# Kernel optimization log

Hardware: AMD Instinct MI355X
Metric: run time of the kernel (lower is better)

The kernel has to match this reference:

```python
import jax, jax.numpy as jnp
import numpy as np

LAM_FACE = 0.1
LAM_HAIR = 0.1
LAM_EYE = 0.1
NBINS = 256


def _denorm255(x):
    # de_norm: (x+1)/2 clamped to [0,1], then *255
    return jnp.clip((x + 1.0) * 0.5, 0.0, 1.0) * 255.0


def _labels_to_mask(m, vals):
    # sum of float indicators, matching (m==v).float() + ... in the original
    out = jnp.zeros(m.shape, jnp.float32)
    for v in vals:
        out = out + (m == v).astype(jnp.float32)
    return out


def _masked_cdf(img_masked, w):
    # img_masked: [3,H,W] values in [0,255] (already multiplied by mask)
    # w: [H,W] bool, one count per nonzero-mask pixel (mirrors mask.nonzero())
    # np.histogram(bins=256, range=(0,255)) -> bin = floor(v*256/255), last bin right-inclusive
    bins = jnp.clip(jnp.floor(img_masked * (256.0 / 255.0)), 0, NBINS - 1).astype(jnp.int32)
    wf = jnp.broadcast_to(w, img_masked.shape).astype(jnp.float32).reshape(3, -1)
    hist = jax.vmap(lambda b, ww: jax.ops.segment_sum(ww, b, num_segments=NBINS))(
        bins.reshape(3, -1), wf)  # [3,256]
    hist = hist / jnp.maximum(hist.sum(axis=1, keepdims=True), 1.0)
    return jnp.cumsum(hist, axis=1)


def _cal_trans(dc, ac):
    # table[i] = first j in 1..255 with dc[i] in [ac[j-1], ac[j]]; else i. table[0]=0, table[255]=255.
    cond = (dc[:, None] >= ac[None, :-1]) & (dc[:, None] <= ac[None, 1:])  # [256,255]
    found = jnp.any(cond, axis=1)
    j = jnp.argmax(cond, axis=1) + 1
    tbl = jnp.where(found, j, jnp.arange(NBINS))
    tbl = tbl.at[0].set(0).at[NBINS - 1].set(NBINS - 1)
    return tbl


def _region_loss(inp, tar, mask_src, mask_tar):
    # inp/tar: [3,H,W] denormed images; mask_*: [H,W] float indicator sums
    w_src = mask_src != 0
    w_tar = mask_tar != 0
    im = inp * mask_src[None]   # input_masked
    tm = tar * mask_tar[None]   # target_masked
    d = _masked_cdf(im, w_src)  # dst CDF per channel
    a = _masked_cdf(tm, w_tar)  # ref CDF per channel
    tables = jax.vmap(_cal_trans)(d, a)  # [3,256] int32
    idx = jnp.clip(im.astype(jnp.int32), 0, NBINS - 1)  # int(value), nonneg so trunc==floor
    looked = jnp.take_along_axis(tables, idx.reshape(3, -1), axis=1).reshape(im.shape)
    matched = jnp.where(w_src[None], looked.astype(im.dtype), im)
    matched = jax.lax.stop_gradient(matched)  # histogram_matching output is requires_grad=False
    return jnp.mean(jnp.abs(im - matched))   # L1Loss over [3,H,W]


def setup_inputs() -> dict:
    key = jax.random.key(0)
    k1, k2, k3, k4 = jax.random.split(key, 4)
    H = 2048
    fake_A = jax.random.normal(k1, (1, 3, H, H), dtype=jnp.float32)
    ref_B = jax.random.normal(k2, (1, 3, H, H), dtype=jnp.float32)
    mask_A = jax.random.randint(k3, (1, 1, H, H), 0, 19, dtype=jnp.int32)
    mask_B = jax.random.randint(k4, (1, 1, H, H), 0, 19, dtype=jnp.int32)
    return {"fake_A": fake_A, "ref_B": ref_B, "mask_A": mask_A, "mask_B": mask_B}


def reference(fake_A, ref_B, mask_A, mask_B):
    ma = mask_A[0, 0]
    mb = mask_B[0, 0]
    # region masks (note: original has a bug, mask_B_face uses (mask_A == 11); kept faithfully)
    mA_face = _labels_to_mask(ma, [1, 10, 14, 7, 8, 11])
    mB_face = _labels_to_mask(mb, [1, 10, 14, 7, 8]) + (ma == 11).astype(jnp.float32)
    mA_hair = _labels_to_mask(ma, [17])
    mB_hair = _labels_to_mask(mb, [17])
    mA_el = _labels_to_mask(ma, [4, 2])
    mA_er = _labels_to_mask(ma, [5, 3])
    mB_el = _labels_to_mask(mb, [4, 2])
    mB_er = _labels_to_mask(mb, [5, 3])
    inp = _denorm255(fake_A[0])
    tar = _denorm255(ref_B[0])
    loss = LAM_FACE * _region_loss(inp, tar, mA_face, mB_face)
    loss = loss + LAM_HAIR * _region_loss(inp, tar, mA_hair, mB_hair)
    loss = loss + LAM_EYE * (_region_loss(inp, tar, mA_el, mB_el)
                             + _region_loss(inp, tar, mA_er, mB_er))
    return loss
```

## Files before the change

kernel.cpp:

```cpp
#include <hip/hip_runtime.h>


typedef unsigned long long u64;
typedef long long s64;

#define NSRC 256
#define M41 ((1ull << 41) - 1)

static constexpr u64 REGA =
    (1ull << (3 * 1)) | (3ull << (3 * 2)) | (4ull << (3 * 3)) |
    (3ull << (3 * 4)) | (4ull << (3 * 5)) | (1ull << (3 * 7)) |
    (1ull << (3 * 8)) | (1ull << (3 * 10)) | (1ull << (3 * 11)) |
    (1ull << (3 * 14)) | (2ull << (3 * 17));
static constexpr u64 REGB =
    (1ull << (3 * 1)) | (3ull << (3 * 2)) | (4ull << (3 * 3)) |
    (3ull << (3 * 4)) | (4ull << (3 * 5)) | (1ull << (3 * 7)) |
    (1ull << (3 * 8)) | (1ull << (3 * 10)) | (1ull << (3 * 14)) |
    (2ull << (3 * 17));

__device__ __forceinline__ float denorm255(float x) {
  float t = (x + 1.0f) * 0.5f;
  t = fminf(fmaxf(t, 0.0f), 1.0f);
  return t * 255.0f;
}

__device__ __forceinline__ int bin_of(float v) {
  int b = (int)(v * (256.0f / 255.0f));
  return b > 255 ? 255 : b;
}

__global__ __launch_bounds__(1024, 8) void hm_kernel(
    const float* __restrict__ fake, const float* __restrict__ refb,
    const int* __restrict__ ma, const int* __restrict__ mb,
    u64* __restrict__ gNS, u64* __restrict__ gT,
    unsigned* __restrict__ ticket, unsigned* __restrict__ ticket2,
    u64* __restrict__ acc, float* __restrict__ out, int npix) {
  __shared__ u64 lds64[6144];
  const int tid = threadIdx.x;
  const int nq = npix >> 2;

  if (blockIdx.x < NSRC) {
    u64* ns = lds64;
    for (int i = tid; i < 6144; i += 1024) ns[i] = 0ull;
    __syncthreads();

    const float4* f0p = (const float4*)fake;
    const float4* f1p = (const float4*)(fake + npix);
    const float4* f2p = (const float4*)(fake + 2 * npix);
    const int4* map = (const int4*)ma;

    for (int q = blockIdx.x * 1024 + tid; q < nq; q += NSRC * 1024) {
      int4 m4 = map[q];
      float4 f0 = f0p[q], f1 = f1p[q], f2 = f2p[q];
      int mm[4] = {m4.x, m4.y, m4.z, m4.w};
      float fa[3][4] = {{f0.x, f0.y, f0.z, f0.w},
                        {f1.x, f1.y, f1.z, f1.w},
                        {f2.x, f2.y, f2.z, f2.w}};
#pragma unroll
      for (int k = 0; k < 4; ++k) {
        unsigned l = (unsigned)mm[k];
        int code = (int)((REGA >> (l + l + l)) & 7u);
        if (code) {
          int base = (code - 1) * 3;
#pragma unroll
          for (int c = 0; c < 3; ++c) {
            float v = denorm255(fa[c][k]);
            int key = (int)v + bin_of(v);
            u64 pack = (1ull << 41) | (u64)(unsigned)(v * 2048.0f);
            atomicAdd(&ns[(base + c) * 512 + key], pack);
          }
        }
      }
    }
    __syncthreads();

    int copy = blockIdx.x & 7;
    int rot = ((blockIdx.x >> 3) & 63) * 8;
    for (int i = tid; i < 6144; i += 1024) {
      int rc = i >> 9, key = ((i & 511) + rot) & 511;
      u64 v = ns[rc * 512 + key];
      if (v) atomicAdd(&gNS[copy * 6144 + rc * 512 + key], v);
    }
  } else {
    unsigned* th0 = (unsigned*)lds64;
    for (int i = tid; i < 12288; i += 1024) th0[i] = 0u;
    __syncthreads();
    unsigned* th = th0 + (tid >> 8) * 3072;

    const float4* r0p = (const float4*)refb;
    const float4* r1p = (const float4*)(refb + npix);
    const float4* r2p = (const float4*)(refb + 2 * npix);
    const int4* map = (const int4*)ma;
    const int4* mbp = (const int4*)mb;

    for (int q = (blockIdx.x - NSRC) * 1024 + tid; q < nq;
         q += (512 - NSRC) * 1024) {
      int4 ma4 = map[q], mb4 = mbp[q];
      float4 r0 = r0p[q], r1 = r1p[q], r2 = r2p[q];
      int mm[4] = {ma4.x, ma4.y, ma4.z, ma4.w};
      int bb[4] = {mb4.x, mb4.y, mb4.z, mb4.w};
      float rr[3][4] = {{r0.x, r0.y, r0.z, r0.w},
                        {r1.x, r1.y, r1.z, r1.w},
                        {r2.x, r2.y, r2.z, r2.w}};
#pragma unroll
      for (int k = 0; k < 4; ++k) {
        unsigned l = (unsigned)bb[k];
        int code = (int)((REGB >> (l + l + l)) & 7u);
        int fval = (code == 1 ? 1 : 0) + (mm[k] == 11 ? 1 : 0);
        if (fval > 0) {
          float fs = (float)fval;
#pragma unroll
          for (int c = 0; c < 3; ++c)
            atomicAdd(&th[c * 256 + bin_of(denorm255(rr[c][k]) * fs)], 1u);
        }
        if (code >= 2) {
          int base = (code - 1) * 3;
#pragma unroll
          for (int c = 0; c < 3; ++c)
            atomicAdd(&th[(base + c) * 256 + bin_of(denorm255(rr[c][k]))], 1u);
        }
      }
    }
    __syncthreads();

    for (int i = tid; i < 3072; i += 1024)
      th0[i] = th0[i] + th0[i + 3072] + th0[i + 6144] + th0[i + 9216];
    __syncthreads();

    int copy = blockIdx.x & 7;
    int rot = ((blockIdx.x >> 3) & 63) * 8;
    for (int i = tid; i < 1536; i += 1024) {
      int rc = i >> 7, p = ((i & 127) + rot) & 127;
      u64 w = (u64)th0[rc * 256 + 2 * p] | ((u64)th0[rc * 256 + 2 * p + 1] << 32);
      if (w) atomicAdd(&gT[copy * 1536 + rc * 128 + p], w);
    }
  }

  asm volatile("s_waitcnt vmcnt(0)" ::: "memory");
  __syncthreads();
  if (tid == 0) atomicAdd(ticket, 1u);
  if (blockIdx.x >= 12) return;

  if (tid == 0) {
    while (__hip_atomic_load(ticket, __ATOMIC_ACQUIRE,
                             __HIP_MEMORY_SCOPE_AGENT) < 512u)
      __builtin_amdgcn_s_sleep(8);
  }
  __syncthreads();

  const int rc = blockIdx.x;
  u64* Sf = lds64;
  unsigned* Nf = (unsigned*)(lds64 + 512);
  unsigned* thA = Nf + 512;
  float* qD = (float*)(thA + 256);
  float* qA = qD + 256;
  float* dcdf = qA + 256;
  float* acdf = dcdf + 256;
  unsigned* rsum = (unsigned*)(acdf + 256);
  s64* red = (s64*)(rsum + 512);

  unsigned hD = 0, wA = 0;
  if (tid < 256) {
    u64 a0 = 0, a1 = 0, w = 0;
#pragma unroll
    for (int cp = 0; cp < 8; ++cp) {
      a0 += __hip_atomic_load(&gNS[cp * 6144 + rc * 512 + 2 * tid],
                              __ATOMIC_RELAXED, __HIP_MEMORY_SCOPE_AGENT);
      a1 += __hip_atomic_load(&gNS[cp * 6144 + rc * 512 + 2 * tid + 1],
                              __ATOMIC_RELAXED, __HIP_MEMORY_SCOPE_AGENT);
    }
    if (tid < 128) {
#pragma unroll
      for (int cp = 0; cp < 8; ++cp)
        w += __hip_atomic_load(&gT[cp * 1536 + rc * 128 + tid],
                               __ATOMIC_RELAXED, __HIP_MEMORY_SCOPE_AGENT);
    }
    Nf[2 * tid] = (unsigned)(a0 >> 41); Sf[2 * tid] = a0 & M41;
    Nf[2 * tid + 1] = (unsigned)(a1 >> 41); Sf[2 * tid + 1] = a1 & M41;
    if (tid < 128) {
      thA[2 * tid] = (unsigned)w;
      thA[2 * tid + 1] = (unsigned)(w >> 32);
    }
  }
  __syncthreads();

  if (tid < 256) {
    hD = Nf[2 * tid] + (tid ? Nf[2 * tid - 1] : 0u);
    wA = thA[tid];
    rsum[tid] = hD;
    rsum[256 + tid] = wA;
  }
  __syncthreads();
  for (int off = 128; off > 0; off >>= 1) {
    if (tid < off) {
      rsum[tid] += rsum[tid + off];
      rsum[256 + tid] += rsum[256 + tid + off];
    }
    __syncthreads();
  }

  if (tid < 256) {
    float sD = fmaxf((float)rsum[0], 1.0f);
    float sA = fmaxf((float)rsum[256], 1.0f);
    qD[tid] = (float)hD / sD;
    qA[tid] = (float)wA / sA;
  }
  __syncthreads();

  if (tid == 0) {
    float run = 0.0f;
    for (int b = 0; b < 256; ++b) { run += qD[b]; dcdf[b] = run; }
  }
  if (tid == 64) {
    float run = 0.0f;
    for (int b = 0; b < 256; ++b) { run += qA[b]; acdf[b] = run; }
  }
  __syncthreads();

  if (tid < 256) {
    int t = tid, tb;
    if (t == 0) tb = 0;
    else if (t == 255) tb = 255;
    else {
      float di = dcdf[t];
      int lo = 1, hi = 255;
      while (lo < hi) {
        int mid = (lo + hi) >> 1;
        if (acdf[mid] >= di) hi = mid; else lo = mid + 1;
      }
      tb = (acdf[lo] >= di && (lo >= 2 || acdf[0] <= di)) ? lo : t;
    }
    unsigned Nb = Nf[2 * t] + Nf[2 * t + 1];
    u64 Sb = Sf[2 * t] + Sf[2 * t + 1];
    s64 nt = (s64)Nb * ((s64)tb << 11);
    red[t] = (tb <= t) ? ((s64)Sb - nt) : (nt - (s64)Sb);
  }
  __syncthreads();
  for (int off = 128; off > 0; off >>= 1) {
    if (tid < off) red[tid] += red[tid + off];
    __syncthreads();
  }

  if (tid == 0) {
    atomicAdd(acc, (u64)red[0]);
    asm volatile("s_waitcnt vmcnt(0)" ::: "memory");
    unsigned t2 = __hip_atomic_fetch_add(ticket2, 1u, __ATOMIC_ACQ_REL,
                                         __HIP_MEMORY_SCOPE_AGENT);
    if (t2 == 11u) {
      s64 total = (s64)__hip_atomic_load(acc, __ATOMIC_ACQUIRE,
                                         __HIP_MEMORY_SCOPE_AGENT);
      out[0] = (float)(0.1 * (double)total / 2048.0 / (3.0 * (double)npix));
    }
  }
}

extern "C" void kernel_launch(void* const* d_in, const int* in_sizes, int n_in,
                              void* d_out, int out_size, void* d_ws, size_t ws_size,
                              hipStream_t stream) {
  const float* fake = (const float*)d_in[0];
  const float* refb = (const float*)d_in[1];
  const int* ma = (const int*)d_in[2];
  const int* mb = (const int*)d_in[3];
  const int npix = in_sizes[2];

  u64* gNS = (u64*)d_ws;
  u64* gT = (u64*)((char*)d_ws + 393216);
  unsigned* ticket = (unsigned*)((char*)d_ws + 491520);
  unsigned* ticket2 = (unsigned*)((char*)d_ws + 491524);
  u64* acc = (u64*)((char*)d_ws + 491528);
  float* out = (float*)d_out;

  hipMemsetAsync(d_ws, 0, 491536, stream);
  hm_kernel<<<512, 1024, 0, stream>>>(fake, refb, ma, mb, gNS, gT, ticket,
                                      ticket2, acc, out, npix);
}
```

Before: 55.18 us.

## Merge source and target histogram work into every block

Stops splitting the grid into separate source-histogram and target-histogram blocks. Every block now builds both the source and target histograms for its pixel range in separate LDS arrays, and a sched_barrier groups all global loads up front. The 4-way replicated target histogram copies in LDS are removed. This balances work across blocks and shares the mask_A load, at the cost of more LDS per block (48KB + 12KB), which may reduce occupancy, and more LDS atomic contention on the unreplicated target histogram.

```diff
diff --git a/kernel.cpp b/kernel.cpp
--- a/kernel.cpp
+++ b/kernel.cpp
@@ -4,7 +4,6 @@
 typedef unsigned long long u64;
 typedef long long s64;
 
-#define NSRC 256
 #define M41 ((1ull << 41) - 1)
 
 static constexpr u64 REGA =
@@ -35,45 +34,73 @@
     u64* __restrict__ gNS, u64* __restrict__ gT,
     unsigned* __restrict__ ticket, unsigned* __restrict__ ticket2,
     u64* __restrict__ acc, float* __restrict__ out, int npix) {
-  __shared__ u64 lds64[6144];
+  __shared__ u64 ns[6144];
+  __shared__ unsigned th[3072];
   const int tid = threadIdx.x;
   const int nq = npix >> 2;
 
-  if (blockIdx.x < NSRC) {
-    u64* ns = lds64;
-    for (int i = tid; i < 6144; i += 1024) ns[i] = 0ull;
-    __syncthreads();
-
-    const float4* f0p = (const float4*)fake;
-    const float4* f1p = (const float4*)(fake + npix);
-    const float4* f2p = (const float4*)(fake + 2 * npix);
-    const int4* map = (const int4*)ma;
-
-    for (int q = blockIdx.x * 1024 + tid; q < nq; q += NSRC * 1024) {
-      int4 m4 = map[q];
-      float4 f0 = f0p[q], f1 = f1p[q], f2 = f2p[q];
-      int mm[4] = {m4.x, m4.y, m4.z, m4.w};
-      float fa[3][4] = {{f0.x, f0.y, f0.z, f0.w},
-                        {f1.x, f1.y, f1.z, f1.w},
-                        {f2.x, f2.y, f2.z, f2.w}};
-#pragma unroll
-      for (int k = 0; k < 4; ++k) {
-        unsigned l = (unsigned)mm[k];
-        int code = (int)((REGA >> (l + l + l)) & 7u);
-        if (code) {
-          int base = (code - 1) * 3;
-#pragma unroll
-          for (int c = 0; c < 3; ++c) {
-            float v = denorm255(fa[c][k]);
-            int key = (int)v + bin_of(v);
-            u64 pack = (1ull << 41) | (u64)(unsigned)(v * 2048.0f);
-            atomicAdd(&ns[(base + c) * 512 + key], pack);
-          }
+  for (int i = tid; i < 6144; i += 1024) ns[i] = 0ull;
+  for (int i = tid; i < 3072; i += 1024) th[i] = 0u;
+  __syncthreads();
+
+  const float4* f0p = (const float4*)fake;
+  const float4* f1p = (const float4*)(fake + npix);
+  const float4* f2p = (const float4*)(fake + 2 * npix);
+  const float4* r0p = (const float4*)refb;
+  const float4* r1p = (const float4*)(refb + npix);
+  const float4* r2p = (const float4*)(refb + 2 * npix);
+  const int4* map = (const int4*)ma;
+  const int4* mbp = (const int4*)mb;
+
+  for (int q = blockIdx.x * 1024 + tid; q < nq; q += 512 * 1024) {
+    int4 m4 = map[q];
+    int4 b4 = mbp[q];
+    float4 f0 = f0p[q], f1 = f1p[q], f2 = f2p[q];
+    float4 r0 = r0p[q], r1 = r1p[q], r2 = r2p[q];
+    __builtin_amdgcn_sched_barrier(0);
+
+    int mm[4] = {m4.x, m4.y, m4.z, m4.w};
+    int bb[4] = {b4.x, b4.y, b4.z, b4.w};
+    float fa[3][4] = {{f0.x, f0.y, f0.z, f0.w},
+                      {f1.x, f1.y, f1.z, f1.w},
+                      {f2.x, f2.y, f2.z, f2.w}};
+    float rr[3][4] = {{r0.x, r0.y, r0.z, r0.w},
+                      {r1.x, r1.y, r1.z, r1.w},
+                      {r2.x, r2.y, r2.z, r2.w}};
+#pragma unroll
+    for (int k = 0; k < 4; ++k) {
+      unsigned la = (unsigned)mm[k];
+      int codeA = (int)((REGA >> (la + la + la)) & 7u);
+      if (codeA) {
+        int base = (codeA - 1) * 3;
+#pragma unroll
+        for (int c = 0; c < 3; ++c) {
+          float v = denorm255(fa[c][k]);
+          int key = (int)v + bin_of(v);
+          u64 pack = (1ull << 41) | (u64)(unsigned)(v * 2048.0f);
+          atomicAdd(&ns[(base + c) * 512 + key], pack);
         }
       }
-    }
-    __syncthreads();
-
+      unsigned lb = (unsigned)bb[k];
+      int codeB = (int)((REGB >> (lb + lb + lb)) & 7u);
+      int fval = (codeB == 1 ? 1 : 0) + (mm[k] == 11 ? 1 : 0);
+      if (fval > 0) {
+        float fs = (float)fval;
+#pragma unroll
+        for (int c = 0; c < 3; ++c)
+          atomicAdd(&th[c * 256 + bin_of(denorm255(rr[c][k]) * fs)], 1u);
+      }
+      if (codeB >= 2) {
+        int base = (codeB - 1) * 3;
+#pragma unroll
+        for (int c = 0; c < 3; ++c)
+          atomicAdd(&th[(base + c) * 256 + bin_of(denorm255(rr[c][k]))], 1u);
+      }
+    }
+  }
+  __syncthreads();
+
+  {
     int copy = blockIdx.x & 7;
     int rot = ((blockIdx.x >> 3) & 63) * 8;
     for (int i = tid; i < 6144; i += 1024) {
@@ -81,57 +108,9 @@
       u64 v = ns[rc * 512 + key];
       if (v) atomicAdd(&gNS[copy * 6144 + rc * 512 + key], v);
     }
-  } else {
-    unsigned* th0 = (unsigned*)lds64;
-    for (int i = tid; i < 12288; i += 1024) th0[i] = 0u;
-    __syncthreads();
-    unsigned* th = th0 + (tid >> 8) * 3072;
-
-    const float4* r0p = (const float4*)refb;
-    const float4* r1p = (const float4*)(refb + npix);
-    const float4* r2p = (const float4*)(refb + 2 * npix);
-    const int4* map = (const int4*)ma;
-    const int4* mbp = (const int4*)mb;
-
-    for (int q = (blockIdx.x - NSRC) * 1024 + tid; q < nq;
-         q += (512 - NSRC) * 1024) {
-      int4 ma4 = map[q], mb4 = mbp[q];
-      float4 r0 = r0p[q], r1 = r1p[q], r2 = r2p[q];
-      int mm[4] = {ma4.x, ma4.y, ma4.z, ma4.w};
-      int bb[4] = {mb4.x, mb4.y, mb4.z, mb4.w};
-      float rr[3][4] = {{r0.x, r0.y, r0.z, r0.w},
-                        {r1.x, r1.y, r1.z, r1.w},
-                        {r2.x, r2.y, r2.z, r2.w}};
-#pragma unroll
-      for (int k = 0; k < 4; ++k) {
-        unsigned l = (unsigned)bb[k];
-        int code = (int)((REGB >> (l + l + l)) & 7u);
-        int fval = (code == 1 ? 1 : 0) + (mm[k] == 11 ? 1 : 0);
-        if (fval > 0) {
-          float fs = (float)fval;
-#pragma unroll
-          for (int c = 0; c < 3; ++c)
-            atomicAdd(&th[c * 256 + bin_of(denorm255(rr[c][k]) * fs)], 1u);
-        }
-        if (code >= 2) {
-          int base = (code - 1) * 3;
-#pragma unroll
-          for (int c = 0; c < 3; ++c)
-            atomicAdd(&th[(base + c) * 256 + bin_of(denorm255(rr[c][k]))], 1u);
-        }
-      }
-    }
-    __syncthreads();
-
-    for (int i = tid; i < 3072; i += 1024)
-      th0[i] = th0[i] + th0[i + 3072] + th0[i + 6144] + th0[i + 9216];
-    __syncthreads();
-
-    int copy = blockIdx.x & 7;
-    int rot = ((blockIdx.x >> 3) & 63) * 8;
     for (int i = tid; i < 1536; i += 1024) {
       int rc = i >> 7, p = ((i & 127) + rot) & 127;
-      u64 w = (u64)th0[rc * 256 + 2 * p] | ((u64)th0[rc * 256 + 2 * p + 1] << 32);
+      u64 w = (u64)th[rc * 256 + 2 * p] | ((u64)th[rc * 256 + 2 * p + 1] << 32);
       if (w) atomicAdd(&gT[copy * 1536 + rc * 128 + p], w);
     }
   }
@@ -149,8 +128,8 @@
   __syncthreads();
 
   const int rc = blockIdx.x;
-  u64* Sf = lds64;
-  unsigned* Nf = (unsigned*)(lds64 + 512);
+  u64* Sf = ns;
+  unsigned* Nf = (unsigned*)(ns + 512);
   unsigned* thA = Nf + 512;
   float* qD = (float*)(thA + 256);
   float* qA = qD + 256;
```

Result: slower. 59.26 us (+7.4%).
